# Kernel tuning notes

Hardware: AMD Instinct MI355X
Metric: run time of the kernel (lower is better)

## Reference

```python
import jax, jax.numpy as jnp
import numpy as np

D, N = 2048, 8192

def setup_inputs() -> dict:
    key = jax.random.key(0)
    k1, k2, k3, k4 = jax.random.split(key, 4)
    return {
        "X_t": jax.random.normal(k1, (D, N), dtype=jnp.float32),
        "W_q": jax.random.normal(k2, (D, D), dtype=jnp.float32),
        "W_k": jax.random.normal(k3, (D, D), dtype=jnp.float32),
        "W_v": jax.random.normal(k4, (D, D), dtype=jnp.float32),
    }

def reference(X_t, W_q, W_k, W_v):
    d = X_t.shape[0]
    Q = W_q @ X_t            # (d, n)
    K = W_v @ X_t            # (d, n)  -- source swaps K/V projections
    V = W_k @ X_t            # (d, n)
    scale = 1.0 / jnp.sqrt(jnp.asarray(d, dtype=X_t.dtype))
    scores = (Q @ K.T) * scale          # (d, d)
    Z = jax.nn.softmax(scores, axis=-1)  # softmax over last dim
    A = Z @ V                            # (d, n)
    return A
```

## Files before the change

kernel.cpp:

```cpp
#include <hip/hip_runtime.h>
#include <math.h>

#define DDIM 2048
#define NDIM 8192
#define NTRI8 36

typedef _Float16 f16;
typedef _Float16 f16x8 __attribute__((ext_vector_type(8)));
typedef _Float16 f16x4 __attribute__((ext_vector_type(4)));
typedef float    f32x4 __attribute__((ext_vector_type(4)));

#define MFMA16(a, b, c) __builtin_amdgcn_mfma_f32_16x16x32_f16(a, b, c, 0, 0, 0)

__device__ __forceinline__ void gload_lds16(const f16* g, f16* l) {
    __builtin_amdgcn_global_load_lds(
        (__attribute__((address_space(1))) const void*)g,
        (__attribute__((address_space(3))) void*)l, 16, 0, 0);
}

#define SBAR() do { __builtin_amdgcn_sched_barrier(0); \
                    __builtin_amdgcn_s_barrier();      \
                    __builtin_amdgcn_sched_barrier(0); } while (0)
#define VMCNT0() asm volatile("s_waitcnt vmcnt(0)" ::: "memory")
#define VMCNT2() asm volatile("s_waitcnt vmcnt(2)" ::: "memory")
#define VMCNT4() asm volatile("s_waitcnt vmcnt(4)" ::: "memory")
#define VMCNT8() asm volatile("s_waitcnt vmcnt(8)" ::: "memory")

__device__ __forceinline__ int xcd_swz(int lin, int n) {
    const int xcd = lin & 7, pos = lin >> 3;
    const int q = n >> 3, r = n & 7;
    return (xcd < r ? xcd * (q + 1) : r * (q + 1) + (xcd - r) * q) + pos;
}

__device__ __forceinline__ int swz(int R, int fo8) {
    return R * 32 + (fo8 ^ (((R >> 1) & 3) << 3));
}

__device__ __forceinline__ void stage_unit(
    const f16* __restrict__ g, int grow0, size_t kelem, int Ktot,
    f16* ldsbase, int tid)
{
#pragma unroll
    for (int i = 0; i < 2; ++i) {
        const int c = tid + i * 512;
        const int row  = c >> 2;
        const int slot = (c & 3) ^ ((c >> 3) & 3);
        gload_lds16(g + (size_t)(grow0 + row) * Ktot + kelem + slot * 8,
                    ldsbase + c * 8);
    }
}

template <bool TRI>
__global__ __launch_bounds__(512, 2) void gemm8_split(
    const f16* __restrict__ Ah_g, const f16* __restrict__ Al_g,
    const f16* __restrict__ Bh_g, const f16* __restrict__ Bl_g,
    float* __restrict__ C, int Mrows, int Ncols, int Ktot, int Kchunk)
{
    __shared__ f16 lds[65536];

    const int tid  = threadIdx.x;
    const int lane = tid & 63;
    const int w    = tid >> 6;
    const int wr   = w >> 2;
    const int wc   = w & 3;
    const int ln15 = lane & 15;
    const int fo8  = (lane >> 4) * 8;

    int row0, col0, nkt;
    size_t kbeg;
    if constexpr (TRI) {
        const int t = xcd_swz(blockIdx.x, NTRI8);
        int i = 0;
        while ((i + 1) * (i + 2) / 2 <= t) ++i;
        const int j = t - i * (i + 1) / 2;
        row0 = i * 256; col0 = j * 256;
        const int z = blockIdx.z;
        const int kb_u = z * 37 - (z > 4 ? z - 4 : 0);
        nkt = (z < 4) ? 37 : 36;
        kbeg = (size_t)kb_u * 32;
        C += ((size_t)z * NTRI8 + t) * (256 * 256);
    } else {
        const int s = xcd_swz(blockIdx.y * gridDim.x + blockIdx.x,
                              gridDim.x * gridDim.y);
        row0 = (s / gridDim.x) * 256;
        col0 = (s % gridDim.x) * 256;
        nkt  = Kchunk / 32;
        kbeg = (size_t)blockIdx.z * Kchunk;
        C += (size_t)blockIdx.z * Mrows * Ncols;
    }

    f32x4 acc[8][4] = {};

    stage_unit(Ah_g, row0, kbeg, Ktot, lds + 0,     tid);
    stage_unit(Al_g, row0, kbeg, Ktot, lds + 8192,  tid);
    stage_unit(Bh_g, col0, kbeg, Ktot, lds + 16384, tid);
    stage_unit(Bl_g, col0, kbeg, Ktot, lds + 24576, tid);
    if (nkt > 1)
        stage_unit(Al_g, row0, kbeg + 32, Ktot, lds + 32768 + 8192, tid);
    VMCNT0();
    SBAR();

    for (int u = 0; u < nkt; ++u) {
        const int cur = (u & 1) * 32768, nxt = ((u + 1) & 1) * 32768;
        const size_t ku = kbeg + (size_t)u * 32;
        f16x8 ah[8], bh[4];

#pragma unroll
        for (int m = 0; m < 8; ++m)
            ah[m] = *(const f16x8*)&lds[cur + swz(wr * 128 + m * 16 + ln15, fo8)];
        bh[0] = *(const f16x8*)&lds[cur + 16384 + swz(wc * 64 +  0 + ln15, fo8)];
        bh[1] = *(const f16x8*)&lds[cur + 16384 + swz(wc * 64 + 16 + ln15, fo8)];
        if (u + 1 < nkt) stage_unit(Bh_g, col0, ku + 32, Ktot, lds + nxt + 16384, tid);
        SBAR();
        __builtin_amdgcn_s_setprio(1);
#pragma unroll
        for (int m = 0; m < 8; ++m) {
            acc[m][0] = MFMA16(ah[m], bh[0], acc[m][0]);
            acc[m][1] = MFMA16(ah[m], bh[1], acc[m][1]);
        }
        __builtin_amdgcn_s_setprio(0);
        SBAR();

        bh[2] = *(const f16x8*)&lds[cur + 16384 + swz(wc * 64 + 32 + ln15, fo8)];
        bh[3] = *(const f16x8*)&lds[cur + 16384 + swz(wc * 64 + 48 + ln15, fo8)];
        if (u + 1 < nkt) stage_unit(Ah_g, row0, ku + 32, Ktot, lds + nxt + 0, tid);
        SBAR();
        __builtin_amdgcn_s_setprio(1);
#pragma unroll
        for (int m = 0; m < 8; ++m) {
            acc[m][2] = MFMA16(ah[m], bh[2], acc[m][2]);
            acc[m][3] = MFMA16(ah[m], bh[3], acc[m][3]);
        }
        __builtin_amdgcn_s_setprio(0);
        SBAR();

        {
            f16x8 al[8];
#pragma unroll
            for (int m = 0; m < 8; ++m)
                al[m] = *(const f16x8*)&lds[cur + 8192 + swz(wr * 128 + m * 16 + ln15, fo8)];
            if (u + 1 < nkt) stage_unit(Bl_g, col0, ku + 32, Ktot, lds + nxt + 24576, tid);
            SBAR();
            __builtin_amdgcn_s_setprio(1);
#pragma unroll
            for (int m = 0; m < 8; ++m)
#pragma unroll
                for (int n = 0; n < 4; ++n)
                    acc[m][n] = MFMA16(al[m], bh[n], acc[m][n]);
            __builtin_amdgcn_s_setprio(0);
        }
        if (u == nkt - 1) { VMCNT0(); } else { VMCNT8(); }
        SBAR();

        {
            f16x8 a2[8], bl[4];
#pragma unroll
            for (int m = 0; m < 8; ++m)
                a2[m] = *(const f16x8*)&lds[cur + swz(wr * 128 + m * 16 + ln15, fo8)];
#pragma unroll
            for (int n = 0; n < 4; ++n)
                bl[n] = *(const f16x8*)&lds[cur + 24576 + swz(wc * 64 + n * 16 + ln15, fo8)];
            if (u + 2 < nkt) stage_unit(Al_g, row0, ku + 64, Ktot, lds + cur + 8192, tid);
            SBAR();
            __builtin_amdgcn_s_setprio(1);
#pragma unroll
            for (int m = 0; m < 8; ++m)
#pragma unroll
                for (int n = 0; n < 4; ++n)
                    acc[m][n] = MFMA16(a2[m], bl[n], acc[m][n]);
            __builtin_amdgcn_s_setprio(0);
        }
        if (u < nkt - 2) { VMCNT4(); }
        else if (u == nkt - 2) { VMCNT2(); }
        SBAR();
    }

    const int rsub = (lane >> 4) * 4;
#pragma unroll
    for (int m = 0; m < 8; ++m)
#pragma unroll
        for (int n = 0; n < 4; ++n)
#pragma unroll
            for (int r = 0; r < 4; ++r) {
                const int cr = wr * 128 + m * 16 + rsub + r;
                const int cc = wc * 64 + n * 16 + ln15;
                if constexpr (TRI)
                    C[(size_t)cr * 256 + cc] = acc[m][n][r];
                else
                    C[(size_t)(row0 + cr) * Ncols + col0 + cc] = acc[m][n][r];
            }
}

__global__ __launch_bounds__(512, 2) void gemm8_nt(
    const f16* __restrict__ A_g, const f16* __restrict__ B_g,
    float* __restrict__ C, int Mrows, int Ncols, int Ktot, int Kchunk)
{
    __shared__ f16 lds[65536];

    const int tid  = threadIdx.x;
    const int lane = tid & 63;
    const int w    = tid >> 6;
    const int wr   = w >> 2;
    const int wc   = w & 3;
    const int ln15 = lane & 15;
    const int fo8  = (lane >> 4) * 8;

    const int s = xcd_swz(blockIdx.y * gridDim.x + blockIdx.x,
                          gridDim.x * gridDim.y);
    const int row0 = (s / gridDim.x) * 256;
    const int col0 = (s % gridDim.x) * 256;
    const int nkt  = Kchunk / 64;
    const size_t kbeg = (size_t)blockIdx.z * Kchunk;
    C += (size_t)blockIdx.z * Mrows * Ncols;

    f32x4 acc[8][4] = {};

    stage_unit(A_g, row0, kbeg,      Ktot, lds + 0,     tid);
    stage_unit(B_g, col0, kbeg,      Ktot, lds + 16384, tid);
    stage_unit(A_g, row0, kbeg + 32, Ktot, lds + 8192,  tid);
    stage_unit(B_g, col0, kbeg + 32, Ktot, lds + 24576, tid);
    VMCNT0();
    SBAR();

    for (int u = 0; u < nkt; ++u) {
        const int cur = (u & 1) * 32768, nxt = ((u + 1) & 1) * 32768;
        const size_t ku = kbeg + (size_t)u * 64;
        f16x8 a[8], b0, b1;

#pragma unroll
        for (int m = 0; m < 8; ++m)
            a[m] = *(const f16x8*)&lds[cur + swz(wr * 128 + m * 16 + ln15, fo8)];
        b0 = *(const f16x8*)&lds[cur + 16384 + swz(wc * 64 +  0 + ln15, fo8)];
        b1 = *(const f16x8*)&lds[cur + 16384 + swz(wc * 64 + 16 + ln15, fo8)];
        if (u + 1 < nkt) stage_unit(A_g, row0, ku + 64, Ktot, lds + nxt + 0, tid);
        SBAR();
        __builtin_amdgcn_s_setprio(1);
#pragma unroll
        for (int m = 0; m < 8; ++m) {
            acc[m][0] = MFMA16(a[m], b0, acc[m][0]);
            acc[m][1] = MFMA16(a[m], b1, acc[m][1]);
        }
        __builtin_amdgcn_s_setprio(0);
        SBAR();

        b0 = *(const f16x8*)&lds[cur + 16384 + swz(wc * 64 + 32 + ln15, fo8)];
        b1 = *(const f16x8*)&lds[cur + 16384 + swz(wc * 64 + 48 + ln15, fo8)];
        if (u + 1 < nkt) stage_unit(B_g, col0, ku + 64, Ktot, lds + nxt + 16384, tid);
        SBAR();
        __builtin_amdgcn_s_setprio(1);
#pragma unroll
        for (int m = 0; m < 8; ++m) {
            acc[m][2] = MFMA16(a[m], b0, acc[m][2]);
            acc[m][3] = MFMA16(a[m], b1, acc[m][3]);
        }
        __builtin_amdgcn_s_setprio(0);
        if (u == nkt - 1) { VMCNT0(); } else { VMCNT4(); }
        SBAR();

#pragma unroll
        for (int m = 0; m < 8; ++m)
            a[m] = *(const f16x8*)&lds[cur + 8192 + swz(wr * 128 + m * 16 + ln15, fo8)];
        b0 = *(const f16x8*)&lds[cur + 24576 + swz(wc * 64 +  0 + ln15, fo8)];
        b1 = *(const f16x8*)&lds[cur + 24576 + swz(wc * 64 + 16 + ln15, fo8)];
        if (u + 1 < nkt) stage_unit(A_g, row0, ku + 96, Ktot, lds + nxt + 8192, tid);
        SBAR();
        __builtin_amdgcn_s_setprio(1);
#pragma unroll
        for (int m = 0; m < 8; ++m) {
            acc[m][0] = MFMA16(a[m], b0, acc[m][0]);
            acc[m][1] = MFMA16(a[m], b1, acc[m][1]);
        }
        __builtin_amdgcn_s_setprio(0);
        SBAR();

        b0 = *(const f16x8*)&lds[cur + 24576 + swz(wc * 64 + 32 + ln15, fo8)];
        b1 = *(const f16x8*)&lds[cur + 24576 + swz(wc * 64 + 48 + ln15, fo8)];
        if (u + 1 < nkt) stage_unit(B_g, col0, ku + 96, Ktot, lds + nxt + 24576, tid);
        SBAR();
        __builtin_amdgcn_s_setprio(1);
#pragma unroll
        for (int m = 0; m < 8; ++m) {
            acc[m][2] = MFMA16(a[m], b0, acc[m][2]);
            acc[m][3] = MFMA16(a[m], b1, acc[m][3]);
        }
        __builtin_amdgcn_s_setprio(0);
        if (u < nkt - 1) { VMCNT4(); }
        SBAR();
    }

    const int rsub = (lane >> 4) * 4;
#pragma unroll
    for (int m = 0; m < 8; ++m)
#pragma unroll
        for (int n = 0; n < 4; ++n)
#pragma unroll
            for (int r = 0; r < 4; ++r)
                C[(size_t)(row0 + wr * 128 + m * 16 + rsub + r) * Ncols
                  + col0 + wc * 64 + n * 16 + ln15] = acc[m][n][r];
}

__global__ __launch_bounds__(256) void split_f32(
    const float* __restrict__ in, f16* __restrict__ hi, f16* __restrict__ lo,
    long n4, float scale)
{
    long i = (long)blockIdx.x * 256 + threadIdx.x;
    if (i >= n4) return;
    float4 x = ((const float4*)in)[i];
    float a = x.x * scale, b = x.y * scale, c = x.z * scale, d = x.w * scale;
    f16x4 h;
    h[0] = (f16)a; h[1] = (f16)b; h[2] = (f16)c; h[3] = (f16)d;
    ((f16x4*)hi)[i] = h;
    if (lo != nullptr) {
        f16x4 l;
        l[0] = (f16)(a - (float)h[0]);
        l[1] = (f16)(b - (float)h[1]);
        l[2] = (f16)(c - (float)h[2]);
        l[3] = (f16)(d - (float)h[3]);
        ((f16x4*)lo)[i] = l;
    }
}

__global__ __launch_bounds__(256) void reduce4_split(
    const float* __restrict__ P, f16* __restrict__ hi, f16* __restrict__ lo,
    long n4, float scale)
{
    long i = (long)blockIdx.x * 256 + threadIdx.x;
    if (i >= n4) return;
    const float4* p = (const float4*)P;
    float4 a = p[i], b = p[i + n4], c = p[i + 2 * n4], d = p[i + 3 * n4];
    float v0 = ((a.x + b.x) + (c.x + d.x)) * scale;
    float v1 = ((a.y + b.y) + (c.y + d.y)) * scale;
    float v2 = ((a.z + b.z) + (c.z + d.z)) * scale;
    float v3 = ((a.w + b.w) + (c.w + d.w)) * scale;
    f16x4 h;
    h[0] = (f16)v0; h[1] = (f16)v1; h[2] = (f16)v2; h[3] = (f16)v3;
    ((f16x4*)hi)[i] = h;
    if (lo != nullptr) {
        f16x4 l;
        l[0] = (f16)(v0 - (float)h[0]);
        l[1] = (f16)(v1 - (float)h[1]);
        l[2] = (f16)(v2 - (float)h[2]);
        l[3] = (f16)(v3 - (float)h[3]);
        ((f16x4*)lo)[i] = l;
    }
}

__global__ __launch_bounds__(256) void reduce7_tri(
    const float* __restrict__ P, f16* __restrict__ hi, f16* __restrict__ lo)
{
    const int t = blockIdx.y;
    int i = 0;
    while ((i + 1) * (i + 2) / 2 <= t) ++i;
    const int j = t - i * (i + 1) / 2;

    const int i4 = blockIdx.x * 256 + threadIdx.x;
    const int r  = i4 >> 6;
    const int c4 = i4 & 63;
    const long zs = (long)NTRI8 * (256 * 256 / 4);
    const float4* q = (const float4*)P + (long)t * (256 * 256 / 4) + i4;

    float v0 = 0.f, v1 = 0.f, v2 = 0.f, v3 = 0.f;
#pragma unroll
    for (int z = 0; z < 7; ++z) {
        float4 a = q[z * zs];
        v0 += a.x; v1 += a.y; v2 += a.z; v3 += a.w;
    }
    f16x4 h;
    h[0] = (f16)v0; h[1] = (f16)v1; h[2] = (f16)v2; h[3] = (f16)v3;
    const size_t o = (size_t)(i * 256 + r) * DDIM + j * 256 + c4 * 4;
    *(f16x4*)&hi[o] = h;
    f16x4 l;
    l[0] = (f16)(v0 - (float)h[0]);
    l[1] = (f16)(v1 - (float)h[1]);
    l[2] = (f16)(v2 - (float)h[2]);
    l[3] = (f16)(v3 - (float)h[3]);
    *(f16x4*)&lo[o] = l;
}

__global__ __launch_bounds__(256) void symm_h(f16* __restrict__ Ghi, f16* __restrict__ Glo)
{
    const int a = blockIdx.y, b = blockIdx.x;
    if (a <= b) return;
    __shared__ f16 tile[64][72];
    const int t = threadIdx.x;
    const int lr = t >> 3, lc8 = t & 7;
    for (int q = 0; q < 2; ++q) {
        f16* G = q ? Glo : Ghi;
        const f16* src = G + ((size_t)a * 64) * DDIM + b * 64;
        f16* dst = G + ((size_t)b * 64) * DDIM + a * 64;
        if (q) __syncthreads();
#pragma unroll
        for (int h = 0; h < 2; ++h) {
            const int r = lr + h * 32;
            f16x8 v = *(const f16x8*)&src[(size_t)r * DDIM + lc8 * 8];
#pragma unroll
            for (int jj = 0; jj < 8; ++jj) tile[r][lc8 * 8 + jj] = v[jj];
        }
        __syncthreads();
#pragma unroll
        for (int h = 0; h < 2; ++h) {
            const int c = lr + h * 32;
            f16x8 v;
#pragma unroll
            for (int jj = 0; jj < 8; ++jj) v[jj] = tile[lc8 * 8 + jj][c];
            *(f16x8*)&dst[(size_t)c * DDIM + lc8 * 8] = v;
        }
    }
}

__global__ __launch_bounds__(256) void transpose_h(
    const f16* __restrict__ in, f16* __restrict__ out, int rows, int cols)
{
    __shared__ f16 tile[64][72];
    const int c0 = blockIdx.x * 64;
    const int r0 = blockIdx.y * 64;
    const int t = threadIdx.x;
    const int lr = t >> 3;
    const int lc8 = t & 7;
#pragma unroll
    for (int h = 0; h < 2; ++h) {
        const int r = lr + h * 32;
        f16x8 v = *(const f16x8*)&in[(size_t)(r0 + r) * cols + c0 + lc8 * 8];
#pragma unroll
        for (int j = 0; j < 8; ++j) tile[r][lc8 * 8 + j] = v[j];
    }
    __syncthreads();
#pragma unroll
    for (int h = 0; h < 2; ++h) {
        const int c = lr + h * 32;
        f16x8 v;
#pragma unroll
        for (int j = 0; j < 8; ++j) v[j] = tile[lc8 * 8 + j][c];
        *(f16x8*)&out[(size_t)(c0 + c) * rows + r0 + lc8 * 8] = v;
    }
}

__global__ __launch_bounds__(256) void softmax_rows4(
    const float* __restrict__ S, f16* __restrict__ Z, int n)
{
    const int row = blockIdx.x;
    const int t = threadIdx.x;
    const int lane = t & 63, wv = t >> 6;
    const long ps = (long)DDIM * DDIM;
    const float* s = S + (size_t)row * n + t * 8;

    float x[8] = {};
#pragma unroll
    for (int q = 0; q < 4; ++q) {
        float4 a = ((const float4*)(s + q * ps))[0];
        float4 b = ((const float4*)(s + q * ps))[1];
        x[0] += a.x; x[1] += a.y; x[2] += a.z; x[3] += a.w;
        x[4] += b.x; x[5] += b.y; x[6] += b.z; x[7] += b.w;
    }

    float m = x[0];
#pragma unroll
    for (int j = 1; j < 8; ++j) m = fmaxf(m, x[j]);
    for (int o = 32; o; o >>= 1) m = fmaxf(m, __shfl_xor(m, o, 64));

    __shared__ float rmax[4], rsum[4];
    if (lane == 0) rmax[wv] = m;
    __syncthreads();
    m = fmaxf(fmaxf(rmax[0], rmax[1]), fmaxf(rmax[2], rmax[3]));

    float e[8], sum = 0.f;
#pragma unroll
    for (int j = 0; j < 8; ++j) { e[j] = expf(x[j] - m); sum += e[j]; }
    for (int o = 32; o; o >>= 1) sum += __shfl_xor(sum, o, 64);
    if (lane == 0) rsum[wv] = sum;
    __syncthreads();
    sum = rsum[0] + rsum[1] + rsum[2] + rsum[3];
    const float rs = 1.0f / sum;

    f16x8 z;
#pragma unroll
    for (int j = 0; j < 8; ++j) z[j] = (f16)(e[j] * rs);
    *(f16x8*)&Z[(size_t)row * n + t * 8] = z;
}

extern "C" void kernel_launch(void* const* d_in, const int* in_sizes, int n_in,
                              void* d_out, int out_size, void* d_ws, size_t ws_size,
                              hipStream_t stream)
{
    const float* X  = (const float*)d_in[0];
    const float* Wq = (const float*)d_in[1];
    const float* Wk = (const float*)d_in[2];
    const float* Wv = (const float*)d_in[3];
    float* out = (float*)d_out;
    char* ws = (char*)d_ws;

    const size_t MiB = 1024 * 1024;
    const size_t NEED = 184 * MiB;
    if (ws_size < NEED) return;

    f16*   Xhi   = (f16*)(ws + 0 * MiB);
    f16*   Xlo   = (f16*)(ws + 32 * MiB);
    f16*   XhiT  = (f16*)(ws + 64 * MiB);
    float* P     = (float*)(ws + 96 * MiB);
    f16*   Ghi   = (f16*)(ws + 160 * MiB);
    f16*   Glo   = (f16*)(ws + 168 * MiB);
    f16*   Z     = (f16*)(ws + 176 * MiB);
    f16*   Wqhi  = (f16*)(ws + 0 * MiB);
    f16*   Wqlo  = (f16*)(ws + 8 * MiB);
    f16*   Wvhi  = (f16*)(ws + 16 * MiB);
    f16*   Wvlo  = (f16*)(ws + 24 * MiB);
    f16*   Wkhi  = (f16*)(ws + 32 * MiB);
    f16*   WkhiT = (f16*)(ws + 40 * MiB);
    f16*   M1hi  = (f16*)(ws + 48 * MiB);
    f16*   M1lo  = (f16*)(ws + 56 * MiB);
    f16*   ZWkhi = (f16*)(ws + 0 * MiB);

    const float scale = 0.022097086912079608f;
    const long n4X = (long)DDIM * NDIM / 4;
    const long n4W = (long)DDIM * DDIM / 4;

    split_f32<<<dim3(n4X / 256), 256, 0, stream>>>(X, Xhi, Xlo, n4X, 1.0f);
    transpose_h<<<dim3(NDIM / 64, DDIM / 64), 256, 0, stream>>>(Xhi, XhiT, DDIM, NDIM);

    gemm8_split<true><<<dim3(NTRI8, 1, 7), 512, 0, stream>>>(
        Xhi, Xlo, Xhi, Xlo, P, DDIM, DDIM, NDIM, 0);
    reduce7_tri<<<dim3(64, NTRI8), 256, 0, stream>>>(P, Ghi, Glo);
    symm_h<<<dim3(32, 32), 256, 0, stream>>>(Ghi, Glo);

    split_f32<<<dim3(n4W / 256), 256, 0, stream>>>(Wq, Wqhi, Wqlo, n4W, 1.0f);
    split_f32<<<dim3(n4W / 256), 256, 0, stream>>>(Wv, Wvhi, Wvlo, n4W, 1.0f);
    split_f32<<<dim3(n4W / 256), 256, 0, stream>>>(Wk, Wkhi, (f16*)nullptr, n4W, 1.0f);
    transpose_h<<<dim3(DDIM / 64, DDIM / 64), 256, 0, stream>>>(Wkhi, WkhiT, DDIM, DDIM);

    gemm8_split<false><<<dim3(8, 8, 4), 512, 0, stream>>>(
        Wqhi, Wqlo, Ghi, Glo, P, DDIM, DDIM, DDIM, DDIM / 4);
    reduce4_split<<<dim3(n4W / 256), 256, 0, stream>>>(P, M1hi, M1lo, n4W, scale);

    gemm8_split<false><<<dim3(8, 8, 4), 512, 0, stream>>>(
        M1hi, M1lo, Wvhi, Wvlo, P, DDIM, DDIM, DDIM, DDIM / 4);
    softmax_rows4<<<dim3(DDIM), 256, 0, stream>>>(P, Z, DDIM);

    gemm8_nt<<<dim3(8, 8, 4), 512, 0, stream>>>(
        Z, WkhiT, P, DDIM, DDIM, DDIM, DDIM / 4);
    reduce4_split<<<dim3(n4W / 256), 256, 0, stream>>>(P, ZWkhi, (f16*)nullptr, n4W, 1.0f);

    gemm8_nt<<<dim3(32, 8, 1), 512, 0, stream>>>(
        ZWkhi, XhiT, out, DDIM, NDIM, DDIM, DDIM);
}
```

Measured before the change: 427.5 us.

## Restructure split-GEMM main loop into three phases and fuse split with transpose

```diff
diff --git a/kernel.cpp b/kernel.cpp
--- a/kernel.cpp
+++ b/kernel.cpp
@@ -22,9 +22,8 @@
                     __builtin_amdgcn_s_barrier();      \
                     __builtin_amdgcn_sched_barrier(0); } while (0)
 #define VMCNT0() asm volatile("s_waitcnt vmcnt(0)" ::: "memory")
-#define VMCNT2() asm volatile("s_waitcnt vmcnt(2)" ::: "memory")
 #define VMCNT4() asm volatile("s_waitcnt vmcnt(4)" ::: "memory")
-#define VMCNT8() asm volatile("s_waitcnt vmcnt(8)" ::: "memory")
+#define VMCNT6() asm volatile("s_waitcnt vmcnt(6)" ::: "memory")
 
 __device__ __forceinline__ int xcd_swz(int lin, int n) {
     const int xcd = lin & 7, pos = lin >> 3;
@@ -95,8 +94,6 @@
     stage_unit(Al_g, row0, kbeg, Ktot, lds + 8192,  tid);
     stage_unit(Bh_g, col0, kbeg, Ktot, lds + 16384, tid);
     stage_unit(Bl_g, col0, kbeg, Ktot, lds + 24576, tid);
-    if (nkt > 1)
-        stage_unit(Al_g, row0, kbeg + 32, Ktot, lds + 32768 + 8192, tid);
     VMCNT0();
     SBAR();
 
@@ -108,37 +105,29 @@
 #pragma unroll
         for (int m = 0; m < 8; ++m)
             ah[m] = *(const f16x8*)&lds[cur + swz(wr * 128 + m * 16 + ln15, fo8)];
-        bh[0] = *(const f16x8*)&lds[cur + 16384 + swz(wc * 64 +  0 + ln15, fo8)];
-        bh[1] = *(const f16x8*)&lds[cur + 16384 + swz(wc * 64 + 16 + ln15, fo8)];
-        if (u + 1 < nkt) stage_unit(Bh_g, col0, ku + 32, Ktot, lds + nxt + 16384, tid);
+#pragma unroll
+        for (int n = 0; n < 4; ++n)
+            bh[n] = *(const f16x8*)&lds[cur + 16384 + swz(wc * 64 + n * 16 + ln15, fo8)];
+        if (u + 1 < nkt) {
+            stage_unit(Bh_g, col0, ku + 32, Ktot, lds + nxt + 16384, tid);
+            stage_unit(Ah_g, row0, ku + 32, Ktot, lds + nxt + 0, tid);
+        }
         SBAR();
         __builtin_amdgcn_s_setprio(1);
 #pragma unroll
-        for (int m = 0; m < 8; ++m) {
-            acc[m][0] = MFMA16(ah[m], bh[0], acc[m][0]);
-            acc[m][1] = MFMA16(ah[m], bh[1], acc[m][1]);
-        }
+        for (int m = 0; m < 8; ++m)
+#pragma unroll
+            for (int n = 0; n < 4; ++n)
+                acc[m][n] = MFMA16(ah[m], bh[n], acc[m][n]);
         __builtin_amdgcn_s_setprio(0);
-        SBAR();
-
-        bh[2] = *(const f16x8*)&lds[cur + 16384 + swz(wc * 64 + 32 + ln15, fo8)];
-        bh[3] = *(const f16x8*)&lds[cur + 16384 + swz(wc * 64 + 48 + ln15, fo8)];
-        if (u + 1 < nkt) stage_unit(Ah_g, row0, ku + 32, Ktot, lds + nxt + 0, tid);
-        SBAR();
-        __builtin_amdgcn_s_setprio(1);
-#pragma unroll
-        for (int m = 0; m < 8; ++m) {
-            acc[m][2] = MFMA16(ah[m], bh[2], acc[m][2]);
-            acc[m][3] = MFMA16(ah[m], bh[3], acc[m][3]);
-        }
-        __builtin_amdgcn_s_setprio(0);
+        if (u == nkt - 1) { VMCNT0(); } else { VMCNT6(); }
         SBAR();
 
         {
-            f16x8 al[8];
-#pragma unroll
-            for (int m = 0; m < 8; ++m)
-                al[m] = *(const f16x8*)&lds[cur + 8192 + swz(wr * 128 + m * 16 + ln15, fo8)];
+            f16x8 bl[4];
+#pragma unroll
+            for (int n = 0; n < 4; ++n)
+                bl[n] = *(const f16x8*)&lds[cur + 24576 + swz(wc * 64 + n * 16 + ln15, fo8)];
             if (u + 1 < nkt) stage_unit(Bl_g, col0, ku + 32, Ktot, lds + nxt + 24576, tid);
             SBAR();
             __builtin_amdgcn_s_setprio(1);
@@ -146,32 +135,28 @@
             for (int m = 0; m < 8; ++m)
 #pragma unroll
                 for (int n = 0; n < 4; ++n)
+                    acc[m][n] = MFMA16(ah[m], bl[n], acc[m][n]);
+            __builtin_amdgcn_s_setprio(0);
+        }
+        if (u + 1 < nkt) { VMCNT6(); }
+        SBAR();
+
+        {
+            f16x8 al[8];
+#pragma unroll
+            for (int m = 0; m < 8; ++m)
+                al[m] = *(const f16x8*)&lds[cur + 8192 + swz(wr * 128 + m * 16 + ln15, fo8)];
+            if (u + 1 < nkt) stage_unit(Al_g, row0, ku + 32, Ktot, lds + nxt + 8192, tid);
+            SBAR();
+            __builtin_amdgcn_s_setprio(1);
+#pragma unroll
+            for (int m = 0; m < 8; ++m)
+#pragma unroll
+                for (int n = 0; n < 4; ++n)
                     acc[m][n] = MFMA16(al[m], bh[n], acc[m][n]);
             __builtin_amdgcn_s_setprio(0);
         }
-        if (u == nkt - 1) { VMCNT0(); } else { VMCNT8(); }
-        SBAR();
-
-        {
-            f16x8 a2[8], bl[4];
-#pragma unroll
-            for (int m = 0; m < 8; ++m)
-                a2[m] = *(const f16x8*)&lds[cur + swz(wr * 128 + m * 16 + ln15, fo8)];
-#pragma unroll
-            for (int n = 0; n < 4; ++n)
-                bl[n] = *(const f16x8*)&lds[cur + 24576 + swz(wc * 64 + n * 16 + ln15, fo8)];
-            if (u + 2 < nkt) stage_unit(Al_g, row0, ku + 64, Ktot, lds + cur + 8192, tid);
-            SBAR();
-            __builtin_amdgcn_s_setprio(1);
-#pragma unroll
-            for (int m = 0; m < 8; ++m)
-#pragma unroll
-                for (int n = 0; n < 4; ++n)
-                    acc[m][n] = MFMA16(a2[m], bl[n], acc[m][n]);
-            __builtin_amdgcn_s_setprio(0);
-        }
-        if (u < nkt - 2) { VMCNT4(); }
-        else if (u == nkt - 2) { VMCNT2(); }
+        if (u + 1 < nkt) { VMCNT4(); }
         SBAR();
     }
 
@@ -317,6 +302,46 @@
         l[2] = (f16)(c - (float)h[2]);
         l[3] = (f16)(d - (float)h[3]);
         ((f16x4*)lo)[i] = l;
+    }
+}
+
+__global__ __launch_bounds__(256) void split_xt(
+    const float* __restrict__ in, f16* __restrict__ hi, f16* __restrict__ lo,
+    f16* __restrict__ hiT, int rows, int cols)
+{
+    __shared__ f16 tile[64][72];
+    const int c0 = blockIdx.x * 64;
+    const int r0 = blockIdx.y * 64;
+    const int t = threadIdx.x;
+    const int lr = t >> 3;
+    const int lc8 = t & 7;
+#pragma unroll
+    for (int h = 0; h < 2; ++h) {
+        const int r = lr + h * 32;
+        const float* src = &in[(size_t)(r0 + r) * cols + c0 + lc8 * 8];
+        float4 a = ((const float4*)src)[0];
+        float4 b = ((const float4*)src)[1];
+        float v[8] = {a.x, a.y, a.z, a.w, b.x, b.y, b.z, b.w};
+        f16x8 hv, lv;
+#pragma unroll
+        for (int j = 0; j < 8; ++j) {
+            hv[j] = (f16)v[j];
+            lv[j] = (f16)(v[j] - (float)hv[j]);
+        }
+        *(f16x8*)&hi[(size_t)(r0 + r) * cols + c0 + lc8 * 8] = hv;
+        if (lo != nullptr)
+            *(f16x8*)&lo[(size_t)(r0 + r) * cols + c0 + lc8 * 8] = lv;
+#pragma unroll
+        for (int j = 0; j < 8; ++j) tile[r][lc8 * 8 + j] = hv[j];
+    }
+    __syncthreads();
+#pragma unroll
+    for (int h = 0; h < 2; ++h) {
+        const int c = lr + h * 32;
+        f16x8 v;
+#pragma unroll
+        for (int j = 0; j < 8; ++j) v[j] = tile[lc8 * 8 + j][c];
+        *(f16x8*)&hiT[(size_t)(c0 + c) * rows + r0 + lc8 * 8] = v;
     }
 }
 
@@ -408,33 +433,6 @@
     }
 }
 
-__global__ __launch_bounds__(256) void transpose_h(
-    const f16* __restrict__ in, f16* __restrict__ out, int rows, int cols)
-{
-    __shared__ f16 tile[64][72];
-    const int c0 = blockIdx.x * 64;
-    const int r0 = blockIdx.y * 64;
-    const int t = threadIdx.x;
-    const int lr = t >> 3;
-    const int lc8 = t & 7;
-#pragma unroll
-    for (int h = 0; h < 2; ++h) {
-        const int r = lr + h * 32;
-        f16x8 v = *(const f16x8*)&in[(size_t)(r0 + r) * cols + c0 + lc8 * 8];
-#pragma unroll
-        for (int j = 0; j < 8; ++j) tile[r][lc8 * 8 + j] = v[j];
-    }
-    __syncthreads();
-#pragma unroll
-    for (int h = 0; h < 2; ++h) {
-        const int c = lr + h * 32;
-        f16x8 v;
-#pragma unroll
-        for (int j = 0; j < 8; ++j) v[j] = tile[lc8 * 8 + j][c];
-        *(f16x8*)&out[(size_t)(c0 + c) * rows + r0 + lc8 * 8] = v;
-    }
-}
-
 __global__ __launch_bounds__(256) void softmax_rows4(
     const float* __restrict__ S, f16* __restrict__ Z, int n)
 {
@@ -511,11 +509,10 @@
     f16*   ZWkhi = (f16*)(ws + 0 * MiB);
 
     const float scale = 0.022097086912079608f;
-    const long n4X = (long)DDIM * NDIM / 4;
     const long n4W = (long)DDIM * DDIM / 4;
 
-    split_f32<<<dim3(n4X / 256), 256, 0, stream>>>(X, Xhi, Xlo, n4X, 1.0f);
-    transpose_h<<<dim3(NDIM / 64, DDIM / 64), 256, 0, stream>>>(Xhi, XhiT, DDIM, NDIM);
+    split_xt<<<dim3(NDIM / 64, DDIM / 64), 256, 0, stream>>>(
+        X, Xhi, Xlo, XhiT, DDIM, NDIM);
 
     gemm8_split<true><<<dim3(NTRI8, 1, 7), 512, 0, stream>>>(
         Xhi, Xlo, Xhi, Xlo, P, DDIM, DDIM, NDIM, 0);
@@ -524,8 +521,8 @@
 
     split_f32<<<dim3(n4W / 256), 256, 0, stream>>>(Wq, Wqhi, Wqlo, n4W, 1.0f);
     split_f32<<<dim3(n4W / 256), 256, 0, stream>>>(Wv, Wvhi, Wvlo, n4W, 1.0f);
-    split_f32<<<dim3(n4W / 256), 256, 0, stream>>>(Wk, Wkhi, (f16*)nullptr, n4W, 1.0f);
-    transpose_h<<<dim3(DDIM / 64, DDIM / 64), 256, 0, stream>>>(Wkhi, WkhiT, DDIM, DDIM);
+    split_xt<<<dim3(DDIM / 64, DDIM / 64), 256, 0, stream>>>(
+        Wk, Wkhi, (f16*)nullptr, WkhiT, DDIM, DDIM);
 
     gemm8_split<false><<<dim3(8, 8, 4), 512, 0, stream>>>(
         Wqhi, Wqlo, Ghi, Glo, P, DDIM, DDIM, DDIM, DDIM / 4);
```

Result: slower. 518.8 us (+21.4%).
